# Optimization experiments

Measured on AMD Instinct MI355X. Metric: run time of the kernel, lower is better.

The kernel has to match this reference:

```python
import jax, jax.numpy as jnp
import numpy as np

N_NODES = 50000
N_EDGES = 800000
IN_DIM = 64
HID_DIM = 64
OUT_DIM = 16
N_RELS = 16
N_BASES = 4


def setup_inputs() -> dict:
    key = jax.random.key(0)
    ks = jax.random.split(key, 11)
    feats = jax.random.normal(ks[0], (N_NODES, IN_DIM), dtype=jnp.float32)
    src = jax.random.randint(ks[1], (N_EDGES,), 0, N_NODES, dtype=jnp.int32)
    dst = jax.random.randint(ks[2], (N_EDGES,), 0, N_NODES, dtype=jnp.int32)
    edge_type = jax.random.randint(ks[3], (N_EDGES,), 0, N_RELS, dtype=jnp.int32)
    edge_norm = jax.random.uniform(ks[4], (N_EDGES,), dtype=jnp.float32)
    # basis-decomposed relation weights: W[r] = sum_b coef[r,b] * bases[b]
    bases1 = jax.random.normal(ks[5], (N_BASES, IN_DIM, HID_DIM), dtype=jnp.float32) * (1.0 / np.sqrt(IN_DIM))
    coef1 = jax.random.normal(ks[6], (N_RELS, N_BASES), dtype=jnp.float32)
    bias1 = jnp.zeros((HID_DIM,), dtype=jnp.float32)
    bases2 = jax.random.normal(ks[7], (N_BASES, HID_DIM, OUT_DIM), dtype=jnp.float32) * (1.0 / np.sqrt(HID_DIM))
    coef2 = jax.random.normal(ks[8], (N_RELS, N_BASES), dtype=jnp.float32)
    bias2 = jnp.zeros((OUT_DIM,), dtype=jnp.float32)
    return {"feats": feats, "src": src, "dst": dst, "edge_type": edge_type,
            "edge_norm": edge_norm, "bases1": bases1, "coef1": coef1, "bias1": bias1,
            "bases2": bases2, "coef2": coef2, "bias2": bias2}


def _rel_graph_conv(x, src, dst, edge_type, edge_norm, bases, coef, bias):
    """One RelGraphConv layer (basis decomposition, low-mem: gather coef, not W)."""
    xs = x[src]                                   # [E, in]  gather source feats
    t = jnp.einsum('ei,bio->ebo', xs, bases)      # [E, B, out] per-basis transform
    c = coef[edge_type]                            # [E, B]   per-edge relation coefs
    msg = jnp.einsum('eb,ebo->eo', c, t)          # [E, out]
    msg = msg * edge_norm[:, None]                # apply edge norm
    h = jax.ops.segment_sum(msg, dst, num_segments=N_NODES)  # scatter-add by dst
    return jax.nn.relu(h + bias)                  # bias + activation (dropout=0, eval)


def reference(feats, src, dst, edge_type, edge_norm, bases1, coef1, bias1, bases2, coef2, bias2):
    h = _rel_graph_conv(feats, src, dst, edge_type, edge_norm, bases1, coef1, bias1)
    h = _rel_graph_conv(h, src, dst, edge_type, edge_norm, bases2, coef2, bias2)
    return h
```

## Files before the change

kernel.cpp:

```cpp
#include <hip/hip_runtime.h>

#define N_NODES 50000
#define N_EDGES 800000

typedef __attribute__((ext_vector_type(8))) short bf16x8;
typedef __attribute__((ext_vector_type(4))) float f32x4;

__device__ __forceinline__ unsigned bf16rne(float x) {
  unsigned u = __float_as_uint(x);
  return (u + 0x7FFFu + ((u >> 16) & 1u)) >> 16;
}
__device__ __forceinline__ unsigned packbf2(float a, float b) {
  return bf16rne(a) | (bf16rne(b) << 16);
}
__device__ __forceinline__ float bflo(unsigned u) { return __uint_as_float(u << 16); }
__device__ __forceinline__ float bfhi(unsigned u) { return __uint_as_float(u & 0xFFFF0000u); }

#define G_HIST 32
#define CHUNK (N_EDGES / G_HIST)
#define NSLICE 4
#define HBINS (N_NODES / NSLICE)
#define NB 512
#define SCAN_BLKS ((N_NODES + NB - 1) / NB)
#define NHIST (G_HIST * NSLICE)
#define NPACK ((N_EDGES + 511) / 512)

__global__ __launch_bounds__(512) void k_prep(
    const float4* __restrict__ feats4, uint2* __restrict__ xbf,
    const float* __restrict__ bases1, const float* __restrict__ bases2,
    unsigned short* __restrict__ b1T, unsigned short* __restrict__ b2p,
    const int* __restrict__ dst, unsigned char* __restrict__ rank,
    unsigned short* __restrict__ bh) {
  __shared__ int hist[HBINS];
  const int bid = blockIdx.x;
  if (bid < NHIST) {
    const int c = bid & (G_HIST - 1);
    const int p = bid >> 5;
    const int e0 = c * CHUNK;
    const int lo = p * HBINS;
    for (int i = threadIdx.x; i < HBINS; i += 512) hist[i] = 0;
    __syncthreads();
    for (int i = threadIdx.x; i < CHUNK; i += 512) {
      const int d = dst[e0 + i] - lo;
      if ((unsigned)d < (unsigned)HBINS)
        rank[e0 + i] = (unsigned char)atomicAdd(&hist[d], 1);
    }
    __syncthreads();
    for (int i = threadIdx.x; i < HBINS; i += 512)
      bh[(size_t)c * N_NODES + lo + i] = (unsigned short)hist[i];
  } else if (bid < NHIST + NPACK) {
    const int i = (bid - NHIST) * 512 + threadIdx.x;
    if (i < N_EDGES) {
      float4 v = feats4[i];
      xbf[i] = make_uint2(packbf2(v.x, v.y), packbf2(v.z, v.w));
    }
  } else {
    for (int idx = threadIdx.x; idx < 64 * 256; idx += 512) {
      int o = idx >> 8, q = idx & 255;
      b1T[idx] = (unsigned short)bf16rne(bases1[q * 64 + o]);
    }
    for (int idx = threadIdx.x; idx < 64 * 64; idx += 512) {
      int j = idx >> 6, k = idx & 63;
      int o = j >> 2, b = j & 3;
      b2p[idx] = (unsigned short)bf16rne(bases2[b * 1024 + k * 16 + o]);
    }
  }
}

__global__ __launch_bounds__(512) void k_scan1(
    unsigned short* __restrict__ bh,
    int* __restrict__ rowp, int* __restrict__ bsum) {
  __shared__ unsigned short tile[G_HIST][NB];
  __shared__ int wsum[8];
  const int tid = threadIdx.x;
  const int n0 = blockIdx.x * NB;
  for (int idx = tid; idx < G_HIST * (NB / 4); idx += 512) {
    const int c = idx >> 7, j = idx & 127;
    const int nloc = 4 * j;
    uint2 u = make_uint2(0u, 0u);
    if (n0 + nloc < N_NODES)
      u = *(const uint2*)(bh + (size_t)c * N_NODES + n0 + nloc);
    *(uint2*)&tile[c][nloc] = u;
  }
  __syncthreads();
  int s = 0;
  for (int c = 0; c < G_HIST; ++c) {
    const int cnt = tile[c][tid];
    tile[c][tid] = (unsigned short)s;
    s += cnt;
  }
  __syncthreads();
  for (int idx = tid; idx < G_HIST * (NB / 4); idx += 512) {
    const int c = idx >> 7, j = idx & 127;
    const int nloc = 4 * j;
    if (n0 + nloc < N_NODES)
      *(uint2*)(bh + (size_t)c * N_NODES + n0 + nloc) = *(uint2*)&tile[c][nloc];
  }
  const int lane = tid & 63, wid = tid >> 6;
  const int v = (n0 + tid < N_NODES) ? s : 0;
  int incl = v;
#pragma unroll
  for (int off = 1; off < 64; off <<= 1) {
    int t = __shfl_up(incl, off, 64);
    if (lane >= off) incl += t;
  }
  if (lane == 63) wsum[wid] = incl;
  __syncthreads();
  if (tid < 8) {
    int wi = wsum[tid];
#pragma unroll
    for (int off = 1; off < 8; off <<= 1) {
      int t = __shfl_up(wi, off, 64);
      if (lane >= off) wi += t;
    }
    wsum[tid] = wi;
  }
  __syncthreads();
  const int woff = (wid > 0) ? wsum[wid - 1] : 0;
  const int incl_all = incl + woff;
  const int n = n0 + tid;
  if (n <= N_NODES) rowp[n] = incl_all - v;
  if (tid == NB - 1) bsum[blockIdx.x] = incl_all;
}

__device__ __forceinline__ int prefix_bsum(const int* __restrict__ bsum,
                                           int b, int lane) {
  int v = 0;
  for (int k = lane; k < b; k += 64) v += bsum[k];
#pragma unroll
  for (int off = 32; off >= 1; off >>= 1) v += __shfl_xor(v, off, 64);
  return v;
}

__global__ __launch_bounds__(256) void k_scatter(
    const int* __restrict__ src, const int* __restrict__ dst,
    const int* __restrict__ ety, const float* __restrict__ enorm,
    const int* __restrict__ rowp, const unsigned char* __restrict__ rank,
    const unsigned short* __restrict__ bh, const int* __restrict__ bsum,
    unsigned* __restrict__ s_edge) {
  __shared__ int sb[128];
  const int tid = threadIdx.x;
  if (tid < 128) sb[tid] = (tid < SCAN_BLKS) ? bsum[tid] : 0;
  __syncthreads();
#pragma unroll
  for (int off = 1; off < 128; off <<= 1) {
    int t = 0;
    if (tid < 128 && tid >= off) t = sb[tid - off];
    __syncthreads();
    if (tid < 128) sb[tid] += t;
    __syncthreads();
  }
  const int e = blockIdx.x * 256 + tid;
  if (e >= N_EDGES) return;
  const int d = dst[e];
  const int b = e / CHUNK;
  const int blk = d >> 9;
  const int boff = blk ? sb[blk - 1] : 0;
  const int pos = rowp[d] + boff + (int)bh[(size_t)b * N_NODES + d] + (int)rank[e];
  unsigned nq = (unsigned)(enorm[e] * 4096.f + 0.5f);
  nq = nq > 4095u ? 4095u : nq;
  s_edge[pos] = (unsigned)src[e] | ((unsigned)ety[e] << 16) | (nq << 20);
}

#define NMSCALE (1.f / 4096.f)

#define ROWB 264
__device__ __forceinline__ void gather_node(
    const unsigned* __restrict__ s_edge, const uint2* __restrict__ xv,
    const float4* __restrict__ coefLDS,
    unsigned short* __restrict__ uA,
    int beg, int end, int m, int lane) {
  const int eslot = lane >> 4, ch4 = lane & 15;
  const int qlen = (end - beg + 3) >> 2;
  int p = beg + eslot * qlen;
  const int pend = min(p + qlen, end);
  float4 a0 = {0, 0, 0, 0}, a1 = {0, 0, 0, 0}, a2 = {0, 0, 0, 0}, a3 = {0, 0, 0, 0};
  for (; p < pend; p += 4) {
    const int nb = pend - p;
    unsigned rec[4];
#pragma unroll
    for (int t = 0; t < 4; ++t) rec[t] = (t < nb) ? s_edge[p + t] : 0u;
    uint2 xp[4];
#pragma unroll
    for (int t = 0; t < 4; ++t) xp[t] = xv[(rec[t] & 0xFFFF) * 16 + ch4];
#pragma unroll
    for (int t = 0; t < 4; ++t) {
      const float nm = (float)(rec[t] >> 20) * NMSCALE;
      const float4 c = coefLDS[(rec[t] >> 16) & 15];
      const float w0 = nm * c.x, w1 = nm * c.y, w2 = nm * c.z, w3 = nm * c.w;
      const float x0 = bflo(xp[t].x), x1 = bfhi(xp[t].x);
      const float x2 = bflo(xp[t].y), x3 = bfhi(xp[t].y);
      a0.x += w0 * x0; a0.y += w0 * x1; a0.z += w0 * x2; a0.w += w0 * x3;
      a1.x += w1 * x0; a1.y += w1 * x1; a1.z += w1 * x2; a1.w += w1 * x3;
      a2.x += w2 * x0; a2.y += w2 * x1; a2.z += w2 * x2; a2.w += w2 * x3;
      a3.x += w3 * x0; a3.y += w3 * x1; a3.z += w3 * x2; a3.w += w3 * x3;
    }
  }
#define RED1(x) x += __shfl_down(x, 32, 64)
  RED1(a0.x); RED1(a0.y); RED1(a0.z); RED1(a0.w);
  RED1(a1.x); RED1(a1.y); RED1(a1.z); RED1(a1.w);
  RED1(a2.x); RED1(a2.y); RED1(a2.z); RED1(a2.w);
  RED1(a3.x); RED1(a3.y); RED1(a3.z); RED1(a3.w);
#undef RED1
  if (eslot < 2) {
    unsigned short* row = uA + (eslot * 16 + m) * ROWB + 4 * ch4;
    *(uint2*)(row + 0 * 64) = make_uint2(packbf2(a0.x, a0.y), packbf2(a0.z, a0.w));
    *(uint2*)(row + 1 * 64) = make_uint2(packbf2(a1.x, a1.y), packbf2(a1.z, a1.w));
    *(uint2*)(row + 2 * 64) = make_uint2(packbf2(a2.x, a2.y), packbf2(a2.z, a2.w));
    *(uint2*)(row + 3 * 64) = make_uint2(packbf2(a3.x, a3.y), packbf2(a3.z, a3.w));
  }
}

__global__ __launch_bounds__(512) void k_l1_fused(
    const int* __restrict__ rowp, const int* __restrict__ bsum,
    const unsigned* __restrict__ s_edge,
    const uint2* __restrict__ xbf, const float* __restrict__ coef1,
    const unsigned short* __restrict__ b1T,
    const float* __restrict__ bias1,
    const unsigned short* __restrict__ b2p,
    uint2* __restrict__ y2bf) {
  __shared__ __align__(16) unsigned short uA[2 * 16 * ROWB];
  __shared__ float coefs[64];
  __shared__ float cmat[16 * 68];
  const int tid = threadIdx.x;
  const int wid = tid >> 6, lane = tid & 63;
  if (tid < 64) coefs[tid] = coef1[tid];
  __syncthreads();
  const int nbase = blockIdx.x * 16;
  const int b0 = nbase >> 9;
  const int boff0 = prefix_bsum(bsum, b0, lane);
  const int bs0 = bsum[b0];
#pragma unroll
  for (int jn = 0; jn < 2; ++jn) {
    const int m = wid * 2 + jn;
    const int node = nbase + m;
    const int beg = rowp[node] + (((node >> 9) == b0) ? boff0 : boff0 + bs0);
    const int end = rowp[node + 1] + ((((node + 1) >> 9) == b0) ? boff0 : boff0 + bs0);
    gather_node(s_edge, xbf, (const float4*)coefs, uA, beg, end, m, lane);
  }
  __syncthreads();
  const int nloc = lane & 15, kgrp = lane >> 4;
  if (wid < 4) {
    f32x4 acc1 = {0.f, 0.f, 0.f, 0.f};
#pragma unroll
    for (int ks = 0; ks < 8; ++ks) {
      const int k0 = ks * 32 + kgrp * 8;
      const bf16x8 b = *(const bf16x8*)&b1T[(wid * 16 + nloc) * 256 + k0];
      const bf16x8 aS0 = *(const bf16x8*)&uA[(0 * 16 + nloc) * ROWB + k0];
      acc1 = __builtin_amdgcn_mfma_f32_16x16x32_bf16(aS0, b, acc1, 0, 0, 0);
      const bf16x8 aS1 = *(const bf16x8*)&uA[(1 * 16 + nloc) * ROWB + k0];
      acc1 = __builtin_amdgcn_mfma_f32_16x16x32_bf16(aS1, b, acc1, 0, 0, 0);
    }
    const int o = wid * 16 + nloc;
    const float bs = bias1[o];
#pragma unroll
    for (int r = 0; r < 4; ++r) {
      const int m = (lane >> 4) * 4 + r;
      cmat[m * 68 + o] = fmaxf(acc1[r] + bs, 0.f);
    }
  }
  __syncthreads();
  f32x4 acc2 = {0.f, 0.f, 0.f, 0.f};
  if (wid < 4) {
#pragma unroll
    for (int ks = 0; ks < 2; ++ks) {
      const int k0 = ks * 32 + kgrp * 8;
      const float4 c0 = *(const float4*)&cmat[nloc * 68 + k0];
      const float4 c1 = *(const float4*)&cmat[nloc * 68 + k0 + 4];
      union { bf16x8 v; unsigned u[4]; } au;
      au.u[0] = packbf2(c0.x, c0.y); au.u[1] = packbf2(c0.z, c0.w);
      au.u[2] = packbf2(c1.x, c1.y); au.u[3] = packbf2(c1.z, c1.w);
      const bf16x8 b = *(const bf16x8*)&b2p[(wid * 16 + nloc) * 64 + k0];
      acc2 = __builtin_amdgcn_mfma_f32_16x16x32_bf16(au.v, b, acc2, 0, 0, 0);
    }
  }
  __syncthreads();
  if (wid < 4) {
#pragma unroll
    for (int r = 0; r < 4; ++r) {
      const int m = (lane >> 4) * 4 + r;
      cmat[m * 68 + wid * 16 + nloc] = acc2[r];
    }
  }
  __syncthreads();
  if (tid < 256) {
    const int nl = tid >> 4, c4 = tid & 15;
    const float* cr = &cmat[nl * 68 + 4 * c4];
    y2bf[(size_t)(nbase + nl) * 16 + c4] =
        make_uint2(packbf2(cr[0], cr[1]), packbf2(cr[2], cr[3]));
  }
}

__global__ __launch_bounds__(512) void k_l2_gather(
    const int* __restrict__ rowp, const int* __restrict__ bsum,
    const unsigned* __restrict__ s_edge,
    const uint4* __restrict__ y2v,
    const float* __restrict__ coef2, const float* __restrict__ bias2,
    float2* __restrict__ out) {
  __shared__ float coefs[64];
  if (threadIdx.x < 64) coefs[threadIdx.x] = coef2[threadIdx.x];
  __syncthreads();
  const float4* coefv = (const float4*)coefs;
  const int wid = threadIdx.x >> 6, lane = threadIdx.x & 63;
  const int eslot = lane >> 3, og = lane & 7;
  const int nbase = blockIdx.x * 16 + wid * 2;
  const int b0 = nbase >> 9;
  const int boff0 = prefix_bsum(bsum, b0, lane);
  const int bs0 = bsum[b0];

  float a0[2] = {0.f, 0.f}, a1[2] = {0.f, 0.f};
  int p[2], pend[2];
#pragma unroll
  for (int m = 0; m < 2; ++m) {
    const int node = nbase + m;
    const int beg = rowp[node] + (((node >> 9) == b0) ? boff0 : boff0 + bs0);
    const int end = rowp[node + 1] + ((((node + 1) >> 9) == b0) ? boff0 : boff0 + bs0);
    const int qlen = (end - beg + 7) >> 3;
    p[m] = beg + eslot * qlen;
    pend[m] = min(p[m] + qlen, end);
  }
  while ((p[0] < pend[0]) | (p[1] < pend[1])) {
    unsigned rec[2][2] = {{0u, 0u}, {0u, 0u}};
#pragma unroll
    for (int m = 0; m < 2; ++m) {
      if (p[m] < pend[m]) rec[m][0] = s_edge[p[m]];
      if (p[m] + 1 < pend[m]) rec[m][1] = s_edge[p[m] + 1];
    }
    uint4 yp[2][2];
#pragma unroll
    for (int m = 0; m < 2; ++m)
#pragma unroll
      for (int t = 0; t < 2; ++t)
        yp[m][t] = y2v[(rec[m][t] & 0xFFFF) * 8 + og];
#pragma unroll
    for (int m = 0; m < 2; ++m)
#pragma unroll
      for (int t = 0; t < 2; ++t) {
        const float nm = (float)(rec[m][t] >> 20) * NMSCALE;
        const float4 c = coefv[(rec[m][t] >> 16) & 15];
        a0[m] += nm * (c.x * bflo(yp[m][t].x) + c.y * bfhi(yp[m][t].x) +
                       c.z * bflo(yp[m][t].y) + c.w * bfhi(yp[m][t].y));
        a1[m] += nm * (c.x * bflo(yp[m][t].z) + c.y * bfhi(yp[m][t].z) +
                       c.z * bflo(yp[m][t].w) + c.w * bfhi(yp[m][t].w));
      }
#pragma unroll
    for (int m = 0; m < 2; ++m) p[m] += 2;
  }
#pragma unroll
  for (int m = 0; m < 2; ++m) {
    a0[m] += __shfl_down(a0[m], 32, 64);
    a0[m] += __shfl_down(a0[m], 16, 64);
    a0[m] += __shfl_down(a0[m], 8, 64);
    a1[m] += __shfl_down(a1[m], 32, 64);
    a1[m] += __shfl_down(a1[m], 16, 64);
    a1[m] += __shfl_down(a1[m], 8, 64);
  }
  if (eslot == 0) {
    const float b0s = bias2[2 * og], b1s = bias2[2 * og + 1];
#pragma unroll
    for (int m = 0; m < 2; ++m) {
      out[(size_t)(nbase + m) * 8 + og] =
          make_float2(fmaxf(a0[m] + b0s, 0.f), fmaxf(a1[m] + b1s, 0.f));
    }
  }
}

extern "C" void kernel_launch(void* const* d_in, const int* in_sizes, int n_in,
                              void* d_out, int out_size, void* d_ws, size_t ws_size,
                              hipStream_t stream) {
  const float* feats  = (const float*)d_in[0];
  const int*   src    = (const int*)d_in[1];
  const int*   dst    = (const int*)d_in[2];
  const int*   etype  = (const int*)d_in[3];
  const float* enorm  = (const float*)d_in[4];
  const float* bases1 = (const float*)d_in[5];
  const float* coef1  = (const float*)d_in[6];
  const float* bias1  = (const float*)d_in[7];
  const float* bases2 = (const float*)d_in[8];
  const float* coef2  = (const float*)d_in[9];
  const float* bias2  = (const float*)d_in[10];

  uint2* xbf    = (uint2*)d_ws;
  uint2* y2bf   = xbf + (size_t)N_NODES * 16;
  unsigned* s_edge = (unsigned*)(y2bf + (size_t)N_NODES * 16);
  unsigned short* bh = (unsigned short*)(s_edge + N_EDGES);
  unsigned short* b1T = bh + (size_t)G_HIST * N_NODES;
  unsigned short* b2p = b1T + 64 * 256;
  int*   rowp   = (int*)(b2p + 64 * 64);
  int*   bsum   = rowp + N_NODES + 1;
  unsigned char* rank = (unsigned char*)(bsum + 128);

  k_prep<<<NHIST + NPACK + 1, 512, 0, stream>>>(
      (const float4*)feats, xbf, bases1, bases2, b1T, b2p, dst, rank, bh);
  k_scan1<<<SCAN_BLKS, 512, 0, stream>>>(bh, rowp, bsum);
  k_scatter<<<(N_EDGES + 255) / 256, 256, 0, stream>>>(
      src, dst, etype, enorm, rowp, rank, bh, bsum, s_edge);
  k_l1_fused<<<N_NODES / 16, 512, 0, stream>>>(rowp, bsum, s_edge, xbf, coef1,
                                               b1T, bias1, b2p, y2bf);
  k_l2_gather<<<N_NODES / 16, 512, 0, stream>>>(rowp, bsum, s_edge,
                                                (const uint4*)y2bf, coef2,
                                                bias2, (float2*)d_out);
}
```

Measured before the change: 186.9 us.

## Precompute per-edge fp32 coef*norm weight tables in scatter instead of packed quantized norm

The scatter kernel now writes two per-edge float4 tables holding edge_norm times the relation coefficients for each layer, and stores the pre-scaled source index in s_edge. The gather kernels load these weights directly and no longer decode a 12-bit quantized norm or look up coefficients in LDS. Out-of-range slots are redirected to a zeroed sentinel entry so loads need no branch. This cuts per-edge ALU and LDS work and removes the norm quantization, but adds about 25 MB of extra writes and reads per call.

```diff
diff --git a/kernel.cpp b/kernel.cpp
--- a/kernel.cpp
+++ b/kernel.cpp
@@ -30,7 +30,9 @@
     const float* __restrict__ bases1, const float* __restrict__ bases2,
     unsigned short* __restrict__ b1T, unsigned short* __restrict__ b2p,
     const int* __restrict__ dst, unsigned char* __restrict__ rank,
-    unsigned short* __restrict__ bh) {
+    unsigned short* __restrict__ bh,
+    unsigned* __restrict__ s_edge, float4* __restrict__ w1tab,
+    float4* __restrict__ w2tab) {
   __shared__ int hist[HBINS];
   const int bid = blockIdx.x;
   if (bid < NHIST) {
@@ -63,6 +65,11 @@
       int j = idx >> 6, k = idx & 63;
       int o = j >> 2, b = j & 3;
       b2p[idx] = (unsigned short)bf16rne(bases2[b * 1024 + k * 16 + o]);
+    }
+    if (threadIdx.x < 4) s_edge[N_EDGES + threadIdx.x] = 0u;
+    if (threadIdx.x == 0) {
+      w1tab[N_EDGES] = make_float4(0.f, 0.f, 0.f, 0.f);
+      w2tab[N_EDGES] = make_float4(0.f, 0.f, 0.f, 0.f);
     }
   }
 }
@@ -137,10 +144,15 @@
     const int* __restrict__ ety, const float* __restrict__ enorm,
     const int* __restrict__ rowp, const unsigned char* __restrict__ rank,
     const unsigned short* __restrict__ bh, const int* __restrict__ bsum,
-    unsigned* __restrict__ s_edge) {
+    const float* __restrict__ coef1, const float* __restrict__ coef2,
+    unsigned* __restrict__ s_edge, float4* __restrict__ w1tab,
+    float4* __restrict__ w2tab) {
   __shared__ int sb[128];
+  __shared__ float cf[128];
   const int tid = threadIdx.x;
   if (tid < 128) sb[tid] = (tid < SCAN_BLKS) ? bsum[tid] : 0;
+  if (tid >= 128 && tid < 192) cf[tid - 128] = coef1[tid - 128];
+  if (tid >= 192) cf[tid - 128] = coef2[tid - 192];
   __syncthreads();
 #pragma unroll
   for (int off = 1; off < 128; off <<= 1) {
@@ -157,17 +169,19 @@
   const int blk = d >> 9;
   const int boff = blk ? sb[blk - 1] : 0;
   const int pos = rowp[d] + boff + (int)bh[(size_t)b * N_NODES + d] + (int)rank[e];
-  unsigned nq = (unsigned)(enorm[e] * 4096.f + 0.5f);
-  nq = nq > 4095u ? 4095u : nq;
-  s_edge[pos] = (unsigned)src[e] | ((unsigned)ety[e] << 16) | (nq << 20);
-}
-
-#define NMSCALE (1.f / 4096.f)
+  const int rel = ety[e];
+  const float nm = enorm[e];
+  const float4 c1 = *(const float4*)&cf[rel * 4];
+  const float4 c2 = *(const float4*)&cf[64 + rel * 4];
+  s_edge[pos] = (unsigned)(src[e] << 4);
+  w1tab[pos] = make_float4(nm * c1.x, nm * c1.y, nm * c1.z, nm * c1.w);
+  w2tab[pos] = make_float4(nm * c2.x, nm * c2.y, nm * c2.z, nm * c2.w);
+}
 
 #define ROWB 264
 __device__ __forceinline__ void gather_node(
-    const unsigned* __restrict__ s_edge, const uint2* __restrict__ xv,
-    const float4* __restrict__ coefLDS,
+    const unsigned* __restrict__ s_edge, const float4* __restrict__ w1tab,
+    const uint2* __restrict__ xv,
     unsigned short* __restrict__ uA,
     int beg, int end, int m, int lane) {
   const int eslot = lane >> 4, ch4 = lane & 15;
@@ -176,24 +190,29 @@
   const int pend = min(p + qlen, end);
   float4 a0 = {0, 0, 0, 0}, a1 = {0, 0, 0, 0}, a2 = {0, 0, 0, 0}, a3 = {0, 0, 0, 0};
   for (; p < pend; p += 4) {
-    const int nb = pend - p;
+    int idx[4];
+#pragma unroll
+    for (int t = 0; t < 4; ++t) {
+      const int q = p + t;
+      idx[t] = (q < pend) ? q : N_EDGES;
+    }
     unsigned rec[4];
 #pragma unroll
-    for (int t = 0; t < 4; ++t) rec[t] = (t < nb) ? s_edge[p + t] : 0u;
+    for (int t = 0; t < 4; ++t) rec[t] = s_edge[idx[t]];
     uint2 xp[4];
 #pragma unroll
-    for (int t = 0; t < 4; ++t) xp[t] = xv[(rec[t] & 0xFFFF) * 16 + ch4];
+    for (int t = 0; t < 4; ++t) xp[t] = xv[rec[t] + ch4];
+    float4 w[4];
+#pragma unroll
+    for (int t = 0; t < 4; ++t) w[t] = w1tab[idx[t]];
 #pragma unroll
     for (int t = 0; t < 4; ++t) {
-      const float nm = (float)(rec[t] >> 20) * NMSCALE;
-      const float4 c = coefLDS[(rec[t] >> 16) & 15];
-      const float w0 = nm * c.x, w1 = nm * c.y, w2 = nm * c.z, w3 = nm * c.w;
       const float x0 = bflo(xp[t].x), x1 = bfhi(xp[t].x);
       const float x2 = bflo(xp[t].y), x3 = bfhi(xp[t].y);
-      a0.x += w0 * x0; a0.y += w0 * x1; a0.z += w0 * x2; a0.w += w0 * x3;
-      a1.x += w1 * x0; a1.y += w1 * x1; a1.z += w1 * x2; a1.w += w1 * x3;
-      a2.x += w2 * x0; a2.y += w2 * x1; a2.z += w2 * x2; a2.w += w2 * x3;
-      a3.x += w3 * x0; a3.y += w3 * x1; a3.z += w3 * x2; a3.w += w3 * x3;
+      a0.x += w[t].x * x0; a0.y += w[t].x * x1; a0.z += w[t].x * x2; a0.w += w[t].x * x3;
+      a1.x += w[t].y * x0; a1.y += w[t].y * x1; a1.z += w[t].y * x2; a1.w += w[t].y * x3;
+      a2.x += w[t].z * x0; a2.y += w[t].z * x1; a2.z += w[t].z * x2; a2.w += w[t].z * x3;
+      a3.x += w[t].w * x0; a3.y += w[t].w * x1; a3.z += w[t].w * x2; a3.w += w[t].w * x3;
     }
   }
 #define RED1(x) x += __shfl_down(x, 32, 64)
@@ -213,19 +232,16 @@
 
 __global__ __launch_bounds__(512) void k_l1_fused(
     const int* __restrict__ rowp, const int* __restrict__ bsum,
-    const unsigned* __restrict__ s_edge,
-    const uint2* __restrict__ xbf, const float* __restrict__ coef1,
+    const unsigned* __restrict__ s_edge, const float4* __restrict__ w1tab,
+    const uint2* __restrict__ xbf,
     const unsigned short* __restrict__ b1T,
     const float* __restrict__ bias1,
     const unsigned short* __restrict__ b2p,
     uint2* __restrict__ y2bf) {
   __shared__ __align__(16) unsigned short uA[2 * 16 * ROWB];
-  __shared__ float coefs[64];
   __shared__ float cmat[16 * 68];
   const int tid = threadIdx.x;
   const int wid = tid >> 6, lane = tid & 63;
-  if (tid < 64) coefs[tid] = coef1[tid];
-  __syncthreads();
   const int nbase = blockIdx.x * 16;
   const int b0 = nbase >> 9;
   const int boff0 = prefix_bsum(bsum, b0, lane);
@@ -236,7 +252,7 @@
     const int node = nbase + m;
     const int beg = rowp[node] + (((node >> 9) == b0) ? boff0 : boff0 + bs0);
     const int end = rowp[node + 1] + ((((node + 1) >> 9) == b0) ? boff0 : boff0 + bs0);
-    gather_node(s_edge, xbf, (const float4*)coefs, uA, beg, end, m, lane);
+    gather_node(s_edge, w1tab, xbf, uA, beg, end, m, lane);
   }
   __syncthreads();
   const int nloc = lane & 15, kgrp = lane >> 4;
@@ -293,14 +309,10 @@
 
 __global__ __launch_bounds__(512) void k_l2_gather(
     const int* __restrict__ rowp, const int* __restrict__ bsum,
-    const unsigned* __restrict__ s_edge,
+    const unsigned* __restrict__ s_edge, const float4* __restrict__ w2tab,
     const uint4* __restrict__ y2v,
-    const float* __restrict__ coef2, const float* __restrict__ bias2,
+    const float* __restrict__ bias2,
     float2* __restrict__ out) {
-  __shared__ float coefs[64];
-  if (threadIdx.x < 64) coefs[threadIdx.x] = coef2[threadIdx.x];
-  __syncthreads();
-  const float4* coefv = (const float4*)coefs;
   const int wid = threadIdx.x >> 6, lane = threadIdx.x & 63;
   const int eslot = lane >> 3, og = lane & 7;
   const int nbase = blockIdx.x * 16 + wid * 2;
@@ -320,28 +332,42 @@
     pend[m] = min(p[m] + qlen, end);
   }
   while ((p[0] < pend[0]) | (p[1] < pend[1])) {
-    unsigned rec[2][2] = {{0u, 0u}, {0u, 0u}};
-#pragma unroll
-    for (int m = 0; m < 2; ++m) {
-      if (p[m] < pend[m]) rec[m][0] = s_edge[p[m]];
-      if (p[m] + 1 < pend[m]) rec[m][1] = s_edge[p[m] + 1];
-    }
+    int idx[2][2];
+#pragma unroll
+    for (int m = 0; m < 2; ++m)
+#pragma unroll
+      for (int t = 0; t < 2; ++t) {
+        const int q = p[m] + t;
+        idx[m][t] = (q < pend[m]) ? q : N_EDGES;
+      }
+    unsigned rec[2][2];
+#pragma unroll
+    for (int m = 0; m < 2; ++m)
+#pragma unroll
+      for (int t = 0; t < 2; ++t) rec[m][t] = s_edge[idx[m][t]];
     uint4 yp[2][2];
 #pragma unroll
     for (int m = 0; m < 2; ++m)
 #pragma unroll
       for (int t = 0; t < 2; ++t)
-        yp[m][t] = y2v[(rec[m][t] & 0xFFFF) * 8 + og];
+        yp[m][t] = y2v[(rec[m][t] >> 1) + og];
+    float4 w[2][2];
 #pragma unroll
     for (int m = 0; m < 2; ++m)
 #pragma unroll
+      for (int t = 0; t < 2; ++t) w[m][t] = w2tab[idx[m][t]];
+#pragma unroll
+    for (int m = 0; m < 2; ++m)
+#pragma unroll
       for (int t = 0; t < 2; ++t) {
-        const float nm = (float)(rec[m][t] >> 20) * NMSCALE;
-        const float4 c = coefv[(rec[m][t] >> 16) & 15];
-        a0[m] += nm * (c.x * bflo(yp[m][t].x) + c.y * bfhi(yp[m][t].x) +
-                       c.z * bflo(yp[m][t].y) + c.w * bfhi(yp[m][t].y));
-        a1[m] += nm * (c.x * bflo(yp[m][t].z) + c.y * bfhi(yp[m][t].z) +
-                       c.z * bflo(yp[m][t].w) + c.w * bfhi(yp[m][t].w));
+        a0[m] += w[m][t].x * bflo(yp[m][t].x);
+        a0[m] += w[m][t].y * bfhi(yp[m][t].x);
+        a0[m] += w[m][t].z * bflo(yp[m][t].y);
+        a0[m] += w[m][t].w * bfhi(yp[m][t].y);
+        a1[m] += w[m][t].x * bflo(yp[m][t].z);
+        a1[m] += w[m][t].y * bfhi(yp[m][t].z);
+        a1[m] += w[m][t].z * bflo(yp[m][t].w);
+        a1[m] += w[m][t].w * bfhi(yp[m][t].w);
       }
 #pragma unroll
     for (int m = 0; m < 2; ++m) p[m] += 2;
@@ -383,21 +409,25 @@
   uint2* xbf    = (uint2*)d_ws;
   uint2* y2bf   = xbf + (size_t)N_NODES * 16;
   unsigned* s_edge = (unsigned*)(y2bf + (size_t)N_NODES * 16);
-  unsigned short* bh = (unsigned short*)(s_edge + N_EDGES);
+  unsigned short* bh = (unsigned short*)(s_edge + N_EDGES + 4);
   unsigned short* b1T = bh + (size_t)G_HIST * N_NODES;
   unsigned short* b2p = b1T + 64 * 256;
-  int*   rowp   = (int*)(b2p + 64 * 64);
+  float4* w1tab = (float4*)(b2p + 64 * 64);
+  float4* w2tab = w1tab + (N_EDGES + 1);
+  int*   rowp   = (int*)(w2tab + (N_EDGES + 1));
   int*   bsum   = rowp + N_NODES + 1;
   unsigned char* rank = (unsigned char*)(bsum + 128);
 
   k_prep<<<NHIST + NPACK + 1, 512, 0, stream>>>(
-      (const float4*)feats, xbf, bases1, bases2, b1T, b2p, dst, rank, bh);
+      (const float4*)feats, xbf, bases1, bases2, b1T, b2p, dst, rank, bh,
+      s_edge, w1tab, w2tab);
   k_scan1<<<SCAN_BLKS, 512, 0, stream>>>(bh, rowp, bsum);
   k_scatter<<<(N_EDGES + 255) / 256, 256, 0, stream>>>(
-      src, dst, etype, enorm, rowp, rank, bh, bsum, s_edge);
-  k_l1_fused<<<N_NODES / 16, 512, 0, stream>>>(rowp, bsum, s_edge, xbf, coef1,
+      src, dst, etype, enorm, rowp, rank, bh, bsum, coef1, coef2,
+      s_edge, w1tab, w2tab);
+  k_l1_fused<<<N_NODES / 16, 512, 0, stream>>>(rowp, bsum, s_edge, w1tab, xbf,
                                                b1T, bias1, b2p, y2bf);
-  k_l2_gather<<<N_NODES / 16, 512, 0, stream>>>(rowp, bsum, s_edge,
-                                                (const uint4*)y2bf, coef2,
-                                                bias2, (float2*)d_out);
-}
+  k_l2_gather<<<N_NODES / 16, 512, 0, stream>>>(rowp, bsum, s_edge, w2tab,
+                                                (const uint4*)y2bf, bias2,
+                                                (float2*)d_out);
+}
```

Result: slower. 206.2 us (+10.3%).
